# Kernel tuning notes

Hardware: AMD Instinct MI355X
Metric: run time of the kernel (lower is better)

## Reference

```python
import jax, jax.numpy as jnp
import numpy as np

B, S, N, F, H, E, L = 16, 64, 128, 16, 64, 1024, 2
NEG_SLOPE = 0.2


def _gat_layer(h, src, tgt, Wl, bl, Wr, br, att, bo):
    # h: [B,S,N,H]; src/tgt: [Et] (edges incl. self-loops)
    xl = jnp.einsum('bsnf,hf->bsnh', h, Wl) + bl
    xr = jnp.einsum('bsnf,hf->bsnh', h, Wr) + br
    e = xl[:, :, src] + xr[:, :, tgt]                       # [B,S,Et,H]
    e = jnp.where(e > 0, e, NEG_SLOPE * e)                  # leaky_relu(0.2)
    a = jnp.einsum('bseh,h->bse', e, att)                   # [B,S,Et]
    # segment softmax over target node (stable)
    m = jnp.full(a.shape[:2] + (N,), -jnp.inf, a.dtype).at[:, :, tgt].max(a)
    p = jnp.exp(a - m[:, :, tgt])
    z = jnp.zeros(a.shape[:2] + (N,), a.dtype).at[:, :, tgt].add(p)
    alpha = p / z[:, :, tgt]
    out = jnp.zeros_like(xl).at[:, :, tgt].add(alpha[..., None] * xl[:, :, src])
    return out + bo


def _forward(x, edge_index, in_W, in_b, gat_Wl, gat_bl, gat_Wr, gat_br,
             gat_att, gat_bias, gru_Wih, gru_Whh, gru_bih, gru_bhh,
             oh_W1, oh_b1, oh_W2, oh_b2, dh_W1, dh_b1, dh_W2, dh_b2):
    ar = jnp.arange(N, dtype=edge_index.dtype)
    ei = jnp.concatenate([edge_index, jnp.stack([ar, ar])], axis=1)  # add self-loops
    src, tgt = ei[0], ei[1]
    h = jnp.einsum('bsnf,hf->bsnh', x, in_W) + in_b          # input_proj
    for l in range(L):
        h = jax.nn.relu(_gat_layer(h, src, tgt, gat_Wl[l], gat_bl[l],
                                   gat_Wr[l], gat_br[l], gat_att[l], gat_bias[l]))
    # [B,S,N,H] -> sequences [B*N, S, H]; GRU, keep last state
    seqs = h.transpose(0, 2, 1, 3).reshape(B * N, S, H)

    def step(hprev, xt):
        gi = xt @ gru_Wih.T + gru_bih
        gh = hprev @ gru_Whh.T + gru_bhh
        ir, iz, inn = jnp.split(gi, 3, axis=-1)
        hr, hz, hn = jnp.split(gh, 3, axis=-1)
        r = jax.nn.sigmoid(ir + hr)
        zz = jax.nn.sigmoid(iz + hz)
        n = jnp.tanh(inn + r * hn)
        hnew = (1 - zz) * n + zz * hprev
        return hnew, None

    h0 = jnp.zeros((B * N, H), h.dtype)
    h_last, _ = jax.lax.scan(step, h0, seqs.transpose(1, 0, 2))
    h_last = h_last.reshape(B, N, H)

    def head(hh, W1, b1, W2, b2):
        return jax.nn.relu(hh @ W1.T + b1) @ W2.T + b2

    order = head(h_last, oh_W1, oh_b1, oh_W2, oh_b2)        # [B,N,1]
    demand = head(h_last, dh_W1, dh_b1, dh_W2, dh_b2)       # [B,N,1]
    return order, demand


def setup_inputs() -> dict:
    key = jax.random.key(0)
    ks = jax.random.split(key, 16)
    def g(i, shp, s=0.05):
        return (jax.random.normal(ks[i], shp) * s).astype(jnp.float32)
    x = jax.random.normal(ks[0], (B, S, N, F), dtype=jnp.float32)
    src = jax.random.randint(ks[1], (E,), 0, N)
    off = jax.random.randint(ks[2], (E,), 1, N)
    edge_index = jnp.stack([src, (src + off) % N]).astype(jnp.int32)  # no self-loops
    zf = lambda shp: jnp.zeros(shp, jnp.float32)
    return dict(
        x=x, edge_index=edge_index,
        in_W=g(3, (H, F)), in_b=zf((H,)),
        gat_Wl=g(4, (L, H, H)), gat_bl=zf((L, H)),
        gat_Wr=g(5, (L, H, H)), gat_br=zf((L, H)),
        gat_att=g(6, (L, H), 0.1), gat_bias=zf((L, H)),
        gru_Wih=g(7, (3 * H, H)), gru_Whh=g(8, (3 * H, H)),
        gru_bih=zf((3 * H,)), gru_bhh=zf((3 * H,)),
        oh_W1=g(9, (H // 2, H)), oh_b1=zf((H // 2,)),
        oh_W2=g(10, (1, H // 2)), oh_b2=zf((1,)),
        dh_W1=g(11, (H // 2, H)), dh_b1=zf((H // 2,)),
        dh_W2=g(12, (1, H // 2)), dh_b2=zf((1,)),
    )


def reference(x, edge_index, in_W, in_b, gat_Wl, gat_bl, gat_Wr, gat_br,
              gat_att, gat_bias, gru_Wih, gru_Whh, gru_bih, gru_bhh,
              oh_W1, oh_b1, oh_W2, oh_b2, dh_W1, dh_b1, dh_W2, dh_b2):
    return _forward(x, edge_index, in_W, in_b, gat_Wl, gat_bl, gat_Wr, gat_br,
                    gat_att, gat_bias, gru_Wih, gru_Whh, gru_bih, gru_bhh,
                    oh_W1, oh_b1, oh_W2, oh_b2, dh_W1, dh_b1, dh_W2, dh_b2)
```

## Files before the change

### kernel.cpp

```cpp
#include <hip/hip_runtime.h>
#include <math.h>

#define BB 16
#define SS 64
#define NN 128
#define FF 16
#define HH 64
#define EE 1024
#define ET 1152
#define LLAYERS 2
#define XPAD 65
#define RT (BB * SS * NN)

__device__ __forceinline__ float readlane_f(float v, int k) {
  return __int_as_float(__builtin_amdgcn_readlane(__float_as_int(v), k));
}
__device__ __forceinline__ unsigned flipf(float f) {
  unsigned u = __float_as_uint(f);
  unsigned mask = (u & 0x80000000u) ? 0xFFFFFFFFu : 0x80000000u;
  return u ^ mask;
}
__device__ __forceinline__ float unflipf(unsigned u) {
  unsigned b = (u & 0x80000000u) ? (u ^ 0x80000000u) : ~u;
  return __uint_as_float(b);
}
__device__ __forceinline__ float sigmoidf_(float x) { return 1.f / (1.f + expf(-x)); }

__global__ void setup_csr_kernel(const int* __restrict__ ei,
                                 int* __restrict__ off,
                                 int* __restrict__ csrc,
                                 int* __restrict__ ctgt) {
  __shared__ int deg[NN], cur[NN], offs[NN + 1];
  int tid = threadIdx.x;
  if (tid < NN) deg[tid] = 0;
  __syncthreads();
  for (int e = tid; e < ET; e += 256) {
    int tg = (e < EE) ? ei[EE + e] : (e - EE);
    atomicAdd(&deg[tg], 1);
  }
  __syncthreads();
  if (tid == 0) {
    int s = 0;
    for (int i = 0; i < NN; ++i) { offs[i] = s; s += deg[i]; }
    offs[NN] = s;
  }
  __syncthreads();
  if (tid < NN) cur[tid] = offs[tid];
  if (tid <= NN) off[tid] = offs[tid];
  __syncthreads();
  for (int e = tid; e < ET; e += 256) {
    int sv, tg;
    if (e < EE) { sv = ei[e]; tg = ei[EE + e]; }
    else        { sv = e - EE; tg = e - EE; }
    int pos = atomicAdd(&cur[tg], 1);
    csrc[pos] = sv;
    ctgt[pos] = tg;
  }
}

__global__ __launch_bounds__(256) void input_proj_kernel(
    const float* __restrict__ x, const float* __restrict__ W,
    const float* __restrict__ bvec, float* __restrict__ h) {
  int lane = threadIdx.x & 63;
  int wid = threadIdx.x >> 6;
  float wreg[FF];
#pragma unroll
  for (int i = 0; i < FF / 4; ++i)
    *(float4*)&wreg[4 * i] = ((const float4*)(W + lane * FF))[i];
  float bias = bvec[lane];
  int row0 = __builtin_amdgcn_readfirstlane((blockIdx.x * 4 + wid) * 32);
#pragma unroll 2
  for (int r = 0; r < 32; ++r) {
    int row = row0 + r;
    const float* xr = x + row * FF;
    float acc = bias;
#pragma unroll
    for (int f = 0; f < FF; ++f) acc += xr[f] * wreg[f];
    h[row * HH + lane] = acc;
  }
}

__global__ __launch_bounds__(128) void xlxr_kernel(
    const float* __restrict__ hin,
    const float* __restrict__ Wl, const float* __restrict__ bl,
    const float* __restrict__ Wr, const float* __restrict__ br,
    float* __restrict__ xl, float* __restrict__ xr) {
  __shared__ float hsh[64 * HH];
  int tid = threadIdx.x;
  int j = tid & 63;
  int w = tid >> 6;
  int row0 = blockIdx.x * 64;
  {
    const float4* src4 = (const float4*)(hin + (size_t)row0 * HH);
    float4* dst4 = (float4*)hsh;
#pragma unroll
    for (int i = 0; i < 8; ++i)
      dst4[i * 128 + tid] = src4[i * 128 + tid];
  }
  __syncthreads();
  const float* W  = w ? Wr : Wl;
  const float* bv = w ? br : bl;
  float* outp     = w ? xr : xl;
  float wreg[HH];
  {
    const float4* ws_ = (const float4*)(W + (size_t)j * HH);
#pragma unroll
    for (int i = 0; i < HH / 4; ++i) *(float4*)&wreg[4 * i] = ws_[i];
  }
  float bias = bv[j];
#pragma unroll 1
  for (int r = 0; r < 64; ++r) {
    float a0 = bias, a1 = 0.f, a2 = 0.f, a3 = 0.f;
#pragma unroll
    for (int k = 0; k < HH; k += 4) {
      float4 hb = *(const float4*)&hsh[r * HH + k];
      a0 += hb.x * wreg[k + 0];
      a1 += hb.y * wreg[k + 1];
      a2 += hb.z * wreg[k + 2];
      a3 += hb.w * wreg[k + 3];
    }
    outp[(size_t)(row0 + r) * HH + j] = (a0 + a1) + (a2 + a3);
  }
}

__global__ __launch_bounds__(256) void gat_edge_kernel(
    const float* __restrict__ xl_g, const float* __restrict__ xr_g,
    float* __restrict__ hout,
    const int* __restrict__ csr_off, const int* __restrict__ csr_src,
    const int* __restrict__ csr_tgt,
    const float* __restrict__ att, const float* __restrict__ bo) {
  __shared__ float xl_sh[NN * XPAD];
  __shared__ float xr_sh[NN * XPAD];
  __shared__ float p_sh[ET];
  __shared__ int st_sh[ET];
  __shared__ unsigned m_sh[NN];
  int tid = threadIdx.x, lane = tid & 63, wid = tid >> 6;
  int base = blockIdx.x * (NN * HH);

#pragma unroll 1
  for (int i = tid * 4; i < NN * HH; i += 256 * 4) {
    int row = i >> 6, h = i & 63;
    float4 vl = *(const float4*)(xl_g + base + i);
    float4 vr = *(const float4*)(xr_g + base + i);
    float* dl = xl_sh + row * XPAD + h;
    float* dr = xr_sh + row * XPAD + h;
    dl[0] = vl.x; dl[1] = vl.y; dl[2] = vl.z; dl[3] = vl.w;
    dr[0] = vr.x; dr[1] = vr.y; dr[2] = vr.z; dr[3] = vr.w;
  }
  for (int i = tid; i < ET; i += 256)
    st_sh[i] = csr_src[i] | (csr_tgt[i] << 16);
  if (tid < NN) m_sh[tid] = 0u;
  __syncthreads();

#pragma unroll 1
  for (int e = tid; e < ET; e += 256) {
    int st = st_sh[e];
    int s = st & 0xffff, tg = st >> 16;
    const float* xlr = xl_sh + s * XPAD;
    const float* xrr = xr_sh + tg * XPAD;
    float a0 = 0.f, a1 = 0.f, a2 = 0.f, a3 = 0.f;
#pragma unroll
    for (int h = 0; h < HH; h += 4) {
      float v0 = xlr[h + 0] + xrr[h + 0]; v0 = (v0 > 0.f) ? v0 : 0.2f * v0;
      float v1 = xlr[h + 1] + xrr[h + 1]; v1 = (v1 > 0.f) ? v1 : 0.2f * v1;
      float v2 = xlr[h + 2] + xrr[h + 2]; v2 = (v2 > 0.f) ? v2 : 0.2f * v2;
      float v3 = xlr[h + 3] + xrr[h + 3]; v3 = (v3 > 0.f) ? v3 : 0.2f * v3;
      a0 += v0 * att[h + 0];
      a1 += v1 * att[h + 1];
      a2 += v2 * att[h + 2];
      a3 += v3 * att[h + 3];
    }
    float a = (a0 + a1) + (a2 + a3);
    p_sh[e] = a;
    atomicMax(&m_sh[tg], flipf(a));
  }
  __syncthreads();

  for (int e = tid; e < ET; e += 256) {
    int tg = st_sh[e] >> 16;
    p_sh[e] = expf(p_sh[e] - unflipf(m_sh[tg]));
  }
  __syncthreads();

  float bo_l = bo[lane];
#pragma unroll 1
  for (int n = wid; n < NN; n += 4) {
    int o0 = __builtin_amdgcn_readfirstlane(csr_off[n]);
    int o1 = __builtin_amdgcn_readfirstlane(csr_off[n + 1]);
    float acc = 0.f, z = 0.f;
    for (int i = o0; i < o1; ++i) {
      float p = p_sh[i];
      int s = st_sh[i] & 0xffff;
      acc += p * xl_sh[s * XPAD + lane];
      z += p;
    }
    float o = acc / z + bo_l;
    hout[base + n * HH + lane] = fmaxf(o, 0.f);
  }
}

__device__ __forceinline__ void gemm_half(
    const float* __restrict__ hin, int base,
    const float* __restrict__ W, const float* __restrict__ bvec,
    float* __restrict__ out_sh, int half, int lane) {
  float wreg[HH];
#pragma unroll
  for (int i = 0; i < HH / 4; ++i)
    *(float4*)&wreg[4 * i] = ((const float4*)(W + lane * HH))[i];
  float bias = bvec[lane];
  int n0 = __builtin_amdgcn_readfirstlane(half * 64);
#pragma unroll 1
  for (int nd = 0; nd < 64; ++nd) {
    int node = n0 + nd;
    const float* hrow = hin + base + node * HH;
    float a0 = bias, a1 = 0.f, a2 = 0.f, a3 = 0.f;
#pragma unroll
    for (int f = 0; f < HH; f += 4) {
      a0 += hrow[f + 0] * wreg[f + 0];
      a1 += hrow[f + 1] * wreg[f + 1];
      a2 += hrow[f + 2] * wreg[f + 2];
      a3 += hrow[f + 3] * wreg[f + 3];
    }
    out_sh[node * HH + lane] = (a0 + a1) + (a2 + a3);
  }
}

__global__ __launch_bounds__(256) void gat_fused_kernel(
    const float* __restrict__ hin, float* __restrict__ hout,
    const int* __restrict__ csr_off, const int* __restrict__ csr_src,
    const int* __restrict__ csr_tgt,
    const float* __restrict__ Wl, const float* __restrict__ bl,
    const float* __restrict__ Wr, const float* __restrict__ br,
    const float* __restrict__ att, const float* __restrict__ bo) {
  __shared__ float xl_sh[NN * HH];
  __shared__ float xr_sh[NN * HH];
  __shared__ float p_sh[ET];
  __shared__ int st_sh[ET];
  __shared__ unsigned m_sh[NN];
  int tid = threadIdx.x, lane = tid & 63, wid = tid >> 6;
  int base = blockIdx.x * (NN * HH);

  for (int i = tid; i < ET; i += 256)
    st_sh[i] = csr_src[i] | (csr_tgt[i] << 16);
  if (tid < NN) m_sh[tid] = 0u;

  if (wid < 2) gemm_half(hin, base, Wl, bl, xl_sh, wid & 1, lane);
  else         gemm_half(hin, base, Wr, br, xr_sh, wid & 1, lane);

  float att_l = att[lane];
  float bo_l = bo[lane];
  __syncthreads();

#pragma unroll 1
  for (int e = wid; e < ET; e += 4) {
    int st = st_sh[e];
    int s = st & 0xffff, tg = st >> 16;
    float v = xl_sh[s * HH + lane] + xr_sh[tg * HH + lane];
    v = (v > 0.f) ? v : 0.2f * v;
    float prod = v * att_l;
#pragma unroll
    for (int mm = 32; mm; mm >>= 1) prod += __shfl_xor(prod, mm);
    if (lane == 0) {
      p_sh[e] = prod;
      atomicMax(&m_sh[tg], flipf(prod));
    }
  }
  __syncthreads();

  for (int e = tid; e < ET; e += 256) {
    int tg = st_sh[e] >> 16;
    p_sh[e] = expf(p_sh[e] - unflipf(m_sh[tg]));
  }
  __syncthreads();

#pragma unroll 1
  for (int n = wid; n < NN; n += 4) {
    int o0 = csr_off[n], o1 = csr_off[n + 1];
    float acc = 0.f, z = 0.f;
    for (int i = o0; i < o1; ++i) {
      float p = p_sh[i];
      int s = st_sh[i] & 0xffff;
      acc += p * xl_sh[s * HH + lane];
      z += p;
    }
    float o = acc / z + bo_l;
    hout[base + n * HH + lane] = fmaxf(o, 0.f);
  }
}

__global__ __launch_bounds__(192) void gi_proj_kernel(
    const float* __restrict__ hin, const float* __restrict__ Wih,
    const float* __restrict__ bih, float* __restrict__ gi) {
  __shared__ float hsh[64 * HH];
  int tid = threadIdx.x;
  int j = tid & 63;
  int g = tid >> 6;
  int row0 = blockIdx.x * 64;
  {
    const float4* src4 = (const float4*)(hin + (size_t)row0 * HH);
    float4* dst4 = (float4*)hsh;
#pragma unroll 1
    for (int i = tid; i < 1024; i += 192)
      dst4[i] = src4[i];
  }
  __syncthreads();
  float wreg[HH];
  {
    const float4* ws_ = (const float4*)(Wih + (size_t)(g * 64 + j) * HH);
#pragma unroll
    for (int i = 0; i < HH / 4; ++i) *(float4*)&wreg[4 * i] = ws_[i];
  }
  float bias = bih[g * 64 + j];
#pragma unroll 1
  for (int r = 0; r < 64; ++r) {
    float a0 = bias, a1 = 0.f, a2 = 0.f, a3 = 0.f;
#pragma unroll
    for (int k = 0; k < HH; k += 4) {
      float4 hb = *(const float4*)&hsh[r * HH + k];
      a0 += hb.x * wreg[k + 0];
      a1 += hb.y * wreg[k + 1];
      a2 += hb.z * wreg[k + 2];
      a3 += hb.w * wreg[k + 3];
    }
    gi[(size_t)(row0 + r) * 192 + g * 64 + j] = (a0 + a1) + (a2 + a3);
  }
}

__global__ __launch_bounds__(64, 2) void gru_rec_kernel(
    const float* __restrict__ gi,
    const float* __restrict__ Whh, const float* __restrict__ bhh,
    const float* __restrict__ oW1, const float* __restrict__ ob1,
    const float* __restrict__ oW2, const float* __restrict__ ob2,
    const float* __restrict__ dW1, const float* __restrict__ db1,
    const float* __restrict__ dW2, const float* __restrict__ db2,
    float* __restrict__ out) {
  int lane = threadIdx.x;
  int seq = blockIdx.x;
  int b = seq >> 7, n = seq & (NN - 1);

  float wr[HH], wz[HH], wn[HH];
  {
    const float4* s0 = (const float4*)(Whh + (size_t)(0 * 64 + lane) * HH);
    const float4* s1 = (const float4*)(Whh + (size_t)(1 * 64 + lane) * HH);
    const float4* s2 = (const float4*)(Whh + (size_t)(2 * 64 + lane) * HH);
#pragma unroll
    for (int i = 0; i < HH / 4; ++i) {
      *(float4*)&wr[4 * i] = s0[i];
      *(float4*)&wz[4 * i] = s1[i];
      *(float4*)&wn[4 * i] = s2[i];
    }
  }
  float br_ = bhh[lane], bz_ = bhh[64 + lane], bn_ = bhh[128 + lane];

  const float* gbase = gi + ((size_t)b * SS * NN + (size_t)n) * 192;
  float gir = gbase[lane], giz = gbase[64 + lane], gin = gbase[128 + lane];
  const float* g1 = gbase + (size_t)NN * 192;
  float pir = g1[lane], piz = g1[64 + lane], pin = g1[128 + lane];
  float hj = 0.f;

#pragma unroll 1
  for (int t = 0; t < SS; ++t) {
    float qir = 0.f, qiz = 0.f, qin = 0.f;
    if (t + 2 < SS) {
      const float* g2 = gbase + (size_t)(t + 2) * NN * 192;
      qir = g2[lane]; qiz = g2[64 + lane]; qin = g2[128 + lane];
    }
    float ar0 = br_, ar1 = 0.f, az0 = bz_, az1 = 0.f, an0 = bn_, an1 = 0.f;
#pragma unroll
    for (int k = 0; k < HH; k += 2) {
      float h0 = readlane_f(hj, k), h1 = readlane_f(hj, k + 1);
      ar0 += h0 * wr[k];     az0 += h0 * wz[k];     an0 += h0 * wn[k];
      ar1 += h1 * wr[k + 1]; az1 += h1 * wz[k + 1]; an1 += h1 * wn[k + 1];
    }
    float r  = sigmoidf_(gir + ar0 + ar1);
    float z  = sigmoidf_(giz + az0 + az1);
    float nn_ = tanhf(gin + r * (an0 + an1));
    hj = (1.f - z) * nn_ + z * hj;
    gir = pir; giz = piz; gin = pin;
    pir = qir; piz = qiz; pin = qin;
  }

  int half = lane >> 5, jp = lane & 31;
  const float* W1 = half ? dW1 : oW1;
  const float* b1 = half ? db1 : ob1;
  const float* W2 = half ? dW2 : oW2;
  const float* b2 = half ? db2 : ob2;
  float wv[HH];
#pragma unroll
  for (int i = 0; i < HH / 4; ++i)
    *(float4*)&wv[4 * i] = ((const float4*)(W1 + jp * HH))[i];
  float acc = b1[jp];
#pragma unroll
  for (int k = 0; k < HH; ++k)
    acc += readlane_f(hj, k) * wv[k];
  float val = fmaxf(acc, 0.f) * W2[jp];
  val += __shfl_down(val, 16, 32);
  val += __shfl_down(val, 8, 32);
  val += __shfl_down(val, 4, 32);
  val += __shfl_down(val, 2, 32);
  val += __shfl_down(val, 1, 32);
  if (jp == 0) out[half * (BB * NN) + seq] = val + b2[0];
}

__global__ __launch_bounds__(192, 3) void gru_fused_kernel(
    const float* __restrict__ hbuf,
    const float* __restrict__ Wih, const float* __restrict__ Whh,
    const float* __restrict__ bih, const float* __restrict__ bhh,
    const float* __restrict__ oW1, const float* __restrict__ ob1,
    const float* __restrict__ oW2, const float* __restrict__ ob2,
    const float* __restrict__ dW1, const float* __restrict__ db1,
    const float* __restrict__ dW2, const float* __restrict__ db2,
    float* __restrict__ out) {
  __shared__ float gi_sh[SS * 3 * HH];
  __shared__ float exch[2][3][HH];

  int lane = threadIdx.x & 63;
  int g = (int)threadIdx.x >> 6;
  int seq = blockIdx.x;
  int b = seq >> 7, n = seq & (NN - 1);
  const float* xbase = hbuf + ((size_t)b * SS * NN + (size_t)n) * HH;

  {
    float w[HH];
    const float4* wsrc = (const float4*)(Wih + (size_t)(g * 64 + lane) * HH);
#pragma unroll
    for (int i = 0; i < HH / 4; ++i) *(float4*)&w[4 * i] = wsrc[i];
    float bias = bih[g * 64 + lane];
#pragma unroll 2
    for (int t = 0; t < SS; ++t) {
      const float* xr = xbase + (size_t)t * NN * HH;
      float a0 = bias, a1 = 0.f, a2 = 0.f, a3 = 0.f;
#pragma unroll
      for (int k = 0; k < HH; k += 4) {
        float4 xb = *(const float4*)(xr + k);
        a0 += xb.x * w[k + 0];
        a1 += xb.y * w[k + 1];
        a2 += xb.z * w[k + 2];
        a3 += xb.w * w[k + 3];
      }
      gi_sh[(t * 3 + g) * HH + lane] = (a0 + a1) + (a2 + a3);
    }
  }

  float whh[HH];
  {
    const float4* wsrc = (const float4*)(Whh + (size_t)(g * 64 + lane) * HH);
#pragma unroll
    for (int i = 0; i < HH / 4; ++i) *(float4*)&whh[4 * i] = wsrc[i];
  }
  float bhg = bhh[g * 64 + lane];
  float hj = 0.f;
  __syncthreads();

#pragma unroll 1
  for (int t = 0; t < SS; ++t) {
    float a0 = bhg, a1 = 0.f, a2 = 0.f, a3 = 0.f;
#pragma unroll
    for (int k = 0; k < HH; k += 4) {
      a0 += readlane_f(hj, k + 0) * whh[k + 0];
      a1 += readlane_f(hj, k + 1) * whh[k + 1];
      a2 += readlane_f(hj, k + 2) * whh[k + 2];
      a3 += readlane_f(hj, k + 3) * whh[k + 3];
    }
    float gh = (a0 + a1) + (a2 + a3);
    int slot = t & 1;
    exch[slot][g][lane] = gh;
    __syncthreads();
    float ghr = exch[slot][0][lane];
    float ghz = exch[slot][1][lane];
    float ghn = exch[slot][2][lane];
    float gir = gi_sh[(t * 3 + 0) * HH + lane];
    float giz = gi_sh[(t * 3 + 1) * HH + lane];
    float gin = gi_sh[(t * 3 + 2) * HH + lane];
    float r  = sigmoidf_(gir + ghr);
    float z  = sigmoidf_(giz + ghz);
    float nn_ = tanhf(gin + r * ghn);
    hj = (1.f - z) * nn_ + z * hj;
  }

  if (g == 0) {
    int half = lane >> 5, jp = lane & 31;
    const float* W1 = half ? dW1 : oW1;
    const float* b1 = half ? db1 : ob1;
    const float* W2 = half ? dW2 : oW2;
    const float* b2 = half ? db2 : ob2;
    float wv[HH];
#pragma unroll
    for (int i = 0; i < HH / 4; ++i)
      *(float4*)&wv[4 * i] = ((const float4*)(W1 + jp * HH))[i];
    float acc = b1[jp];
#pragma unroll
    for (int k = 0; k < HH; ++k)
      acc += readlane_f(hj, k) * wv[k];
    float val = fmaxf(acc, 0.f) * W2[jp];
    val += __shfl_down(val, 16, 32);
    val += __shfl_down(val, 8, 32);
    val += __shfl_down(val, 4, 32);
    val += __shfl_down(val, 2, 32);
    val += __shfl_down(val, 1, 32);
    if (jp == 0) out[half * (BB * NN) + seq] = val + b2[0];
  }
}

extern "C" void kernel_launch(void* const* d_in, const int* in_sizes, int n_in,
                              void* d_out, int out_size, void* d_ws, size_t ws_size,
                              hipStream_t stream) {
  const float* x       = (const float*)d_in[0];
  const int*   ei      = (const int*)d_in[1];
  const float* in_W    = (const float*)d_in[2];
  const float* in_b    = (const float*)d_in[3];
  const float* gat_Wl  = (const float*)d_in[4];
  const float* gat_bl  = (const float*)d_in[5];
  const float* gat_Wr  = (const float*)d_in[6];
  const float* gat_br  = (const float*)d_in[7];
  const float* gat_att = (const float*)d_in[8];
  const float* gat_bias= (const float*)d_in[9];
  const float* gru_Wih = (const float*)d_in[10];
  const float* gru_Whh = (const float*)d_in[11];
  const float* gru_bih = (const float*)d_in[12];
  const float* gru_bhh = (const float*)d_in[13];
  const float* oh_W1   = (const float*)d_in[14];
  const float* oh_b1   = (const float*)d_in[15];
  const float* oh_W2   = (const float*)d_in[16];
  const float* oh_b2   = (const float*)d_in[17];
  const float* dh_W1   = (const float*)d_in[18];
  const float* dh_b1   = (const float*)d_in[19];
  const float* dh_W2   = (const float*)d_in[20];
  const float* dh_b2   = (const float*)d_in[21];
  float* out = (float*)d_out;

  char* ws = (char*)d_ws;
  size_t hfloats = (size_t)BB * SS * NN * HH;
  float* hbuf = (float*)ws;
  size_t off_csr = hfloats * sizeof(float);
  size_t off_buf = off_csr + (160 + 2 * ET) * sizeof(int);
  off_buf = (off_buf + 255) & ~(size_t)255;
  int* csr_off = (int*)(ws + off_csr);
  int* csr_src = csr_off + 160;
  int* csr_tgt = csr_src + ET;
  float* xlbuf = (float*)(ws + off_buf);
  float* xrbuf = xlbuf + hfloats;
  size_t need_gat = off_buf + 2 * hfloats * sizeof(float);
  bool big_gat = (ws_size >= need_gat);
  float* gibuf = (float*)(ws + off_buf);
  size_t need_gru = off_buf + (size_t)RT * 192 * sizeof(float);
  bool big_gru = (ws_size >= need_gru);

  setup_csr_kernel<<<1, 256, 0, stream>>>(ei, csr_off, csr_src, csr_tgt);
  input_proj_kernel<<<(BB * SS * NN) / (4 * 32), 256, 0, stream>>>(x, in_W, in_b, hbuf);
  for (int l = 0; l < LLAYERS; ++l) {
    if (big_gat) {
      xlxr_kernel<<<RT / 64, 128, 0, stream>>>(
          hbuf, gat_Wl + l * HH * HH, gat_bl + l * HH,
          gat_Wr + l * HH * HH, gat_br + l * HH, xlbuf, xrbuf);
      gat_edge_kernel<<<BB * SS, 256, 0, stream>>>(
          xlbuf, xrbuf, hbuf, csr_off, csr_src, csr_tgt,
          gat_att + l * HH, gat_bias + l * HH);
    } else {
      gat_fused_kernel<<<BB * SS, 256, 0, stream>>>(
          hbuf, hbuf, csr_off, csr_src, csr_tgt,
          gat_Wl + l * HH * HH, gat_bl + l * HH,
          gat_Wr + l * HH * HH, gat_br + l * HH,
          gat_att + l * HH, gat_bias + l * HH);
    }
  }
  if (big_gru) {
    gi_proj_kernel<<<RT / 64, 192, 0, stream>>>(hbuf, gru_Wih, gru_bih, gibuf);
    gru_rec_kernel<<<BB * NN, 64, 0, stream>>>(
        gibuf, gru_Whh, gru_bhh,
        oh_W1, oh_b1, oh_W2, oh_b2, dh_W1, dh_b1, dh_W2, dh_b2, out);
  } else {
    gru_fused_kernel<<<BB * NN, 192, 0, stream>>>(
        hbuf, gru_Wih, gru_Whh, gru_bih, gru_bhh,
        oh_W1, oh_b1, oh_W2, oh_b2, dh_W1, dh_b1, dh_W2, dh_b2, out);
  }
}
```

Baseline: 603.5 us.

## Swap projection kernels to per-row registers with uniform scalar weight loads

Restructures the xl/xr and GRU input projection kernels so each lane keeps one input row in registers and loops over output columns. Weight rows become wave-uniform reads that can use scalar loads, replacing the per-iteration LDS reads of the input. The GRU projection drops to 128 threads with 96 outputs per wave. In exchange, each lane now writes its outputs at a 64- or 192-float stride, which risks uncoalesced global stores.

```diff
diff --git a/kernel.cpp b/kernel.cpp
--- a/kernel.cpp
+++ b/kernel.cpp
@@ -10,6 +10,7 @@
 #define ET 1152
 #define LLAYERS 2
 #define XPAD 65
+#define HPAD 68
 #define RT (BB * SS * NN)
 
 __device__ __forceinline__ float readlane_f(float v, int k) {
@@ -85,41 +86,42 @@
     const float* __restrict__ Wl, const float* __restrict__ bl,
     const float* __restrict__ Wr, const float* __restrict__ br,
     float* __restrict__ xl, float* __restrict__ xr) {
-  __shared__ float hsh[64 * HH];
+  __shared__ float hsh[64 * HPAD];
   int tid = threadIdx.x;
-  int j = tid & 63;
-  int w = tid >> 6;
+  int l = tid & 63;
+  int w = __builtin_amdgcn_readfirstlane(tid >> 6);
   int row0 = blockIdx.x * 64;
   {
     const float4* src4 = (const float4*)(hin + (size_t)row0 * HH);
-    float4* dst4 = (float4*)hsh;
-#pragma unroll
-    for (int i = 0; i < 8; ++i)
-      dst4[i * 128 + tid] = src4[i * 128 + tid];
-  }
-  __syncthreads();
+#pragma unroll
+    for (int i = 0; i < 8; ++i) {
+      int idx = i * 128 + tid;
+      int r = idx >> 4, c = idx & 15;
+      *(float4*)&hsh[r * HPAD + c * 4] = src4[idx];
+    }
+  }
+  __syncthreads();
+  float hreg[HH];
+#pragma unroll
+  for (int c = 0; c < 16; ++c)
+    *(float4*)&hreg[4 * c] = *(const float4*)&hsh[l * HPAD + c * 4];
+
   const float* W  = w ? Wr : Wl;
   const float* bv = w ? br : bl;
   float* outp     = w ? xr : xl;
-  float wreg[HH];
-  {
-    const float4* ws_ = (const float4*)(W + (size_t)j * HH);
-#pragma unroll
-    for (int i = 0; i < HH / 4; ++i) *(float4*)&wreg[4 * i] = ws_[i];
-  }
-  float bias = bv[j];
-#pragma unroll 1
-  for (int r = 0; r < 64; ++r) {
-    float a0 = bias, a1 = 0.f, a2 = 0.f, a3 = 0.f;
+  size_t outbase = (size_t)(row0 + l) * HH;
+#pragma unroll 1
+  for (int j = 0; j < HH; ++j) {
+    const float* wrow = W + (size_t)j * HH;
+    float a0 = bv[j], a1 = 0.f, a2 = 0.f, a3 = 0.f;
 #pragma unroll
     for (int k = 0; k < HH; k += 4) {
-      float4 hb = *(const float4*)&hsh[r * HH + k];
-      a0 += hb.x * wreg[k + 0];
-      a1 += hb.y * wreg[k + 1];
-      a2 += hb.z * wreg[k + 2];
-      a3 += hb.w * wreg[k + 3];
-    }
-    outp[(size_t)(row0 + r) * HH + j] = (a0 + a1) + (a2 + a3);
+      a0 += hreg[k + 0] * wrow[k + 0];
+      a1 += hreg[k + 1] * wrow[k + 1];
+      a2 += hreg[k + 2] * wrow[k + 2];
+      a3 += hreg[k + 3] * wrow[k + 3];
+    }
+    outp[outbase + j] = (a0 + a1) + (a2 + a3);
   }
 }
 
@@ -288,41 +290,43 @@
   }
 }
 
-__global__ __launch_bounds__(192) void gi_proj_kernel(
+__global__ __launch_bounds__(128) void gi_proj_kernel(
     const float* __restrict__ hin, const float* __restrict__ Wih,
     const float* __restrict__ bih, float* __restrict__ gi) {
-  __shared__ float hsh[64 * HH];
+  __shared__ float hsh[64 * HPAD];
   int tid = threadIdx.x;
-  int j = tid & 63;
-  int g = tid >> 6;
+  int l = tid & 63;
+  int w = __builtin_amdgcn_readfirstlane(tid >> 6);
   int row0 = blockIdx.x * 64;
   {
     const float4* src4 = (const float4*)(hin + (size_t)row0 * HH);
-    float4* dst4 = (float4*)hsh;
-#pragma unroll 1
-    for (int i = tid; i < 1024; i += 192)
-      dst4[i] = src4[i];
-  }
-  __syncthreads();
-  float wreg[HH];
-  {
-    const float4* ws_ = (const float4*)(Wih + (size_t)(g * 64 + j) * HH);
-#pragma unroll
-    for (int i = 0; i < HH / 4; ++i) *(float4*)&wreg[4 * i] = ws_[i];
-  }
-  float bias = bih[g * 64 + j];
-#pragma unroll 1
-  for (int r = 0; r < 64; ++r) {
-    float a0 = bias, a1 = 0.f, a2 = 0.f, a3 = 0.f;
+#pragma unroll
+    for (int i = 0; i < 8; ++i) {
+      int idx = i * 128 + tid;
+      int r = idx >> 4, c = idx & 15;
+      *(float4*)&hsh[r * HPAD + c * 4] = src4[idx];
+    }
+  }
+  __syncthreads();
+  float hreg[HH];
+#pragma unroll
+  for (int c = 0; c < 16; ++c)
+    *(float4*)&hreg[4 * c] = *(const float4*)&hsh[l * HPAD + c * 4];
+
+  size_t outbase = (size_t)(row0 + l) * 192;
+  int j0 = w * 96;
+#pragma unroll 1
+  for (int j = j0; j < j0 + 96; ++j) {
+    const float* wrow = Wih + (size_t)j * HH;
+    float a0 = bih[j], a1 = 0.f, a2 = 0.f, a3 = 0.f;
 #pragma unroll
     for (int k = 0; k < HH; k += 4) {
-      float4 hb = *(const float4*)&hsh[r * HH + k];
-      a0 += hb.x * wreg[k + 0];
-      a1 += hb.y * wreg[k + 1];
-      a2 += hb.z * wreg[k + 2];
-      a3 += hb.w * wreg[k + 3];
-    }
-    gi[(size_t)(row0 + r) * 192 + g * 64 + j] = (a0 + a1) + (a2 + a3);
+      a0 += hreg[k + 0] * wrow[k + 0];
+      a1 += hreg[k + 1] * wrow[k + 1];
+      a2 += hreg[k + 2] * wrow[k + 2];
+      a3 += hreg[k + 3] * wrow[k + 3];
+    }
+    gi[outbase + j] = (a0 + a1) + (a2 + a3);
   }
 }
 
@@ -565,7 +569,7 @@
     }
   }
   if (big_gru) {
-    gi_proj_kernel<<<RT / 64, 192, 0, stream>>>(hbuf, gru_Wih, gru_bih, gibuf);
+    gi_proj_kernel<<<RT / 64, 128, 0, stream>>>(hbuf, gru_Wih, gru_bih, gibuf);
     gru_rec_kernel<<<BB * NN, 64, 0, stream>>>(
         gibuf, gru_Whh, gru_bhh,
         oh_W1, oh_b1, oh_W2, oh_b2, dh_W1, dh_b1, dh_W2, dh_b2, out);
```

After: 777.3 us. 28.8% more time.
